# Kernel optimization log

Measured on AMD Instinct MI355X. Metric: run time of the kernel, lower is better.

Reference implementation:

```python
import jax, jax.numpy as jnp
import numpy as np

NUM_HEADS = 16
NEG = -1e9

def setup_inputs() -> dict:
    key = jax.random.key(0)
    ks = jax.random.split(key, 5)
    B, S, D = 4, 2048, 1024
    scale = 1.0 / np.sqrt(D)
    return {
        "x": jax.random.normal(ks[0], (B, S, D), dtype=jnp.float32),
        "WQ": jax.random.normal(ks[1], (D, D), dtype=jnp.float32) * scale,
        "WK": jax.random.normal(ks[2], (D, D), dtype=jnp.float32) * scale,
        "WV": jax.random.normal(ks[3], (D, D), dtype=jnp.float32) * scale,
        "WO": jax.random.normal(ks[4], (D, D), dtype=jnp.float32) * scale,
    }

def _split_heads(t, h):
    # [..., s, h*d] -> [..., h, s, d]
    *lead, s, hd = t.shape
    return jnp.swapaxes(t.reshape(*lead, s, h, hd // h), -3, -2)

def reference(x, WQ, WK, WV, WO):
    h = NUM_HEADS
    S = x.shape[-2]
    # Linear stores weight [out, in]; y = x @ W^T
    Q = _split_heads(x @ WQ.T, h)  # [b,h,s,dk]
    K = _split_heads(x @ WK.T, h)
    V = _split_heads(x @ WV.T, h)
    dk = Q.shape[-1]
    scores = jnp.einsum('bhqd,bhkd->bhqk', Q, K) / jnp.sqrt(jnp.float32(dk))
    causal = jnp.tril(jnp.ones((S, S), dtype=bool))  # allowed positions
    scores = jnp.where(causal, scores, NEG)
    # explicit stable softmax (matches source)
    m = jnp.max(scores, axis=-1, keepdims=True)
    e = jnp.exp(scores - m)
    attn = e / jnp.sum(e, axis=-1, keepdims=True)
    out = jnp.einsum('bhqk,bhkd->bhqd', attn, V)  # [b,h,s,dv]
    out = jnp.swapaxes(out, -3, -2).reshape(*x.shape[:-1], -1)  # [b,s,h*dv]
    return out @ WO.T
```

## Files before the change

kernel.cpp:

```cpp
#include <hip/hip_runtime.h>
#include <stdint.h>
#include <math.h>

typedef __attribute__((ext_vector_type(8))) short bf16x8;
typedef __attribute__((ext_vector_type(4))) short v4s;
typedef __attribute__((ext_vector_type(4))) float f32x4;
typedef __attribute__((ext_vector_type(4))) unsigned short u16x4;
typedef __attribute__((ext_vector_type(2))) unsigned int u32x2;

#define MFMA16(a,b,c)   __builtin_amdgcn_mfma_f32_16x16x32_bf16((a),(b),(c),0,0,0)
#define MFMA16K(a,b,c)  __builtin_amdgcn_mfma_f32_16x16x16bf16_1k((a),(b),(c),0,0,0)

static __device__ __forceinline__ void gld_lds16(const void* g, void* l) {
  __builtin_amdgcn_global_load_lds(
      (const __attribute__((address_space(1))) unsigned int*)g,
      (__attribute__((address_space(3))) unsigned int*)l,
      16, 0, 0);
}

static __device__ __forceinline__ unsigned short f2bf(float f) {
  unsigned int u = __builtin_bit_cast(unsigned int, f);
  return (unsigned short)((u + 0x8000u) >> 16);
}

__global__ __launch_bounds__(256) void cvt_kernel(const float* __restrict__ in,
                                                  unsigned short* __restrict__ out,
                                                  int n4) {
  int i = blockIdx.x * blockDim.x + threadIdx.x;
  int stride = gridDim.x * blockDim.x;
  for (; i < n4; i += stride) {
    float4 v = ((const float4*)in)[i];
    u16x4 o;
    o.x = f2bf(v.x); o.y = f2bf(v.y); o.z = f2bf(v.z); o.w = f2bf(v.w);
    ((u16x4*)out)[i] = o;
  }
}

__global__ __launch_bounds__(256) void cvt4_kernel(const float* __restrict__ w0,
                                                   const float* __restrict__ w1,
                                                   const float* __restrict__ w2,
                                                   const float* __restrict__ w3,
                                                   unsigned short* __restrict__ out) {
  const float* in = (blockIdx.y == 0) ? w0 : (blockIdx.y == 1) ? w1
                  : (blockIdx.y == 2) ? w2 : w3;
  unsigned short* o = out + (size_t)blockIdx.y * 1048576;
  int i = blockIdx.x * blockDim.x + threadIdx.x;
  int stride = gridDim.x * blockDim.x;
  for (; i < 1048576/4; i += stride) {
    float4 v = ((const float4*)in)[i];
    u16x4 t;
    t.x = f2bf(v.x); t.y = f2bf(v.y); t.z = f2bf(v.z); t.w = f2bf(v.w);
    ((u16x4*)o)[i] = t;
  }
}

template<int MODE, typename CT>
__device__ __forceinline__ void gemm_bt_tile(const unsigned short* __restrict__ A,
                                             const unsigned short* __restrict__ Bt,
                                             CT* __restrict__ C,
                                             int m0, int n0)
{
  __shared__ __align__(16) unsigned short As[128*32];
  __shared__ __align__(16) unsigned short Bs[128*32];
  const int tid  = threadIdx.x;
  const int w    = tid >> 6, lane = tid & 63;
  const int quad = lane >> 4, c0 = lane & 15;
  const int wm   = w >> 1, wn = w & 1;

  const unsigned short* ga[2];
  const unsigned short* gb[2];
  int ldsoff[2];
  #pragma unroll
  for (int i = 0; i < 2; ++i) {
    int f = i*4096 + w*1024 + lane*16;
    int r = f >> 6;
    int q = (f >> 4) & 3;
    ga[i] = A  + (m0 + r)*1024 + q*8;
    gb[i] = Bt + (n0 + r)*1024 + q*8;
    ldsoff[i] = i*4096 + w*1024;
  }

  int aAddr[4], bAddr[4];
  #pragma unroll
  for (int t = 0; t < 4; ++t) {
    aAddr[t] = (wm*64 + t*16 + c0)*64 + quad*16;
    bAddr[t] = (wn*64 + t*16 + c0)*64 + quad*16;
  }

  f32x4 acc[4][4];
  #pragma unroll
  for (int i = 0; i < 4; ++i)
    #pragma unroll
    for (int j = 0; j < 4; ++j)
      acc[i][j] = (f32x4){0.f, 0.f, 0.f, 0.f};

  for (int kt = 0; kt < 32; ++kt) {
    __syncthreads();
    #pragma unroll
    for (int i = 0; i < 2; ++i) {
      gld_lds16(ga[i] + kt*32, (char*)As + ldsoff[i]);
      gld_lds16(gb[i] + kt*32, (char*)Bs + ldsoff[i]);
    }
    __syncthreads();

    bf16x8 af[4], bfr[4];
    #pragma unroll
    for (int t = 0; t < 4; ++t) af[t]  = *(const bf16x8*)((const char*)As + aAddr[t]);
    #pragma unroll
    for (int t = 0; t < 4; ++t) bfr[t] = *(const bf16x8*)((const char*)Bs + bAddr[t]);

    #pragma unroll
    for (int mt = 0; mt < 4; ++mt)
      #pragma unroll
      for (int nt = 0; nt < 4; ++nt)
        acc[mt][nt] = MFMA16(af[mt], bfr[nt], acc[mt][nt]);
  }

  const float scl = (MODE == 3) ? 0.1803368801f : 1.0f;
  #pragma unroll
  for (int mt = 0; mt < 4; ++mt) {
    #pragma unroll
    for (int nt = 0; nt < 4; ++nt) {
      if (MODE == 2) {
        u16x4 pk;
        #pragma unroll
        for (int r = 0; r < 4; ++r) pk[r] = f2bf(acc[mt][nt][r]);
        int s0 = m0 + wm*64 + mt*16 + quad*4;
        int gc = n0 + wn*64 + nt*16 + c0;
        int b = s0 >> 11, ss = s0 & 2047;
        int h = gc >> 6, d = gc & 63;
        *(u16x4*)((unsigned short*)C + (size_t)(((b << 4) + h)*64 + d)*2048 + ss) = pk;
      } else {
        #pragma unroll
        for (int r = 0; r < 4; ++r) {
          int gr = m0 + wm*64 + mt*16 + quad*4 + r;
          int gc = n0 + wn*64 + nt*16 + c0;
          if (MODE == 0 || MODE == 3) {
            int b = gr >> 11, s = gr & 2047;
            int h = gc >> 6, d = gc & 63;
            ((unsigned short*)C)[(((b << 4) + h)*2048 + s)*64 + d] = f2bf(acc[mt][nt][r] * scl);
          } else {
            ((float*)C)[gr*1024 + gc] = acc[mt][nt][r];
          }
        }
      }
    }
  }
}

__global__ __launch_bounds__(256) void qkv_kernel(
    const unsigned short* __restrict__ X,
    const unsigned short* __restrict__ WQ, const unsigned short* __restrict__ WK,
    const unsigned short* __restrict__ WV,
    unsigned short* __restrict__ Q, unsigned short* __restrict__ K,
    unsigned short* __restrict__ V)
{
  if (blockIdx.z == 2) {
    gemm_bt_tile<2>(X, WV, V, blockIdx.x*128, blockIdx.y*128);
  } else if (blockIdx.z == 0) {
    gemm_bt_tile<3>(X, WQ, Q, blockIdx.x*128, blockIdx.y*128);
  } else {
    gemm_bt_tile<0>(X, WK, K, blockIdx.x*128, blockIdx.y*128);
  }
}

__global__ __launch_bounds__(256) void proj_kernel(
    const unsigned short* __restrict__ A,
    const unsigned short* __restrict__ WO,
    float* __restrict__ C)
{
  gemm_bt_tile<1>(A, WO, C, blockIdx.x*128, blockIdx.y*128);
}

__global__ __launch_bounds__(256) void attn_kernel(
    const unsigned short* __restrict__ Q,
    const unsigned short* __restrict__ K,
    const unsigned short* __restrict__ Vt,
    unsigned short* __restrict__ O)
{
  __shared__ __align__(16) unsigned short VtL[2][64*128];

  const int tid  = threadIdx.x;
  const int w    = tid >> 6, lane = tid & 63;
  const int quad = lane >> 4, c0 = lane & 15;
  const int bx = blockIdx.x, bh = blockIdx.y;

  const unsigned short* Qh = Q  + (size_t)bh*2048*64;
  const unsigned short* Kh = K  + (size_t)bh*2048*64;
  const unsigned short* Vh = Vt + (size_t)bh*64*2048;

  const unsigned short* vga[4];
  int vldsoff[4];
  #pragma unroll
  for (int i = 0; i < 4; ++i) {
    int cid = i*256 + tid;
    int r = cid >> 4, q = cid & 15;
    int gq = q ^ (r & 15);
    vga[i] = Vh + (size_t)r*2048 + gq*8;
    vldsoff[i] = i*4096 + w*1024;
  }

  const int b = bh >> 4, h = bh & 15;
  bf16x8 kreg[8][2];

  #define ATTN_MK_BODY(mk, Vb, DIAG)                                              \
  {                                                                               \
    f32x4 s0 = (f32x4){0.f,0.f,0.f,0.f}, s1 = (f32x4){0.f,0.f,0.f,0.f};           \
    _Pragma("unroll")                                                             \
    for (int ks = 0; ks < 2; ++ks) {                                              \
      s0 = MFMA16(kreg[mk][ks], qf[0][ks], s0);                                   \
      s1 = MFMA16(kreg[mk][ks], qf[1][ks], s1);                                   \
    }                                                                             \
    if (DIAG) {                                                                   \
      _Pragma("unroll")                                                           \
      for (int r = 0; r < 4; ++r) {                                               \
        int kk = (mk)*16 + quad*4 + r;                                            \
        if (kk > w*32 + c0)      s0[r] = -1e30f;                                  \
        if (kk > w*32 + 16 + c0) s1[r] = -1e30f;                                  \
      }                                                                           \
    }                                                                             \
    float p00 = __builtin_amdgcn_exp2f(s0[0]), p01 = __builtin_amdgcn_exp2f(s0[1]); \
    float p02 = __builtin_amdgcn_exp2f(s0[2]), p03 = __builtin_amdgcn_exp2f(s0[3]); \
    float p10 = __builtin_amdgcn_exp2f(s1[0]), p11 = __builtin_amdgcn_exp2f(s1[1]); \
    float p12 = __builtin_amdgcn_exp2f(s1[2]), p13 = __builtin_amdgcn_exp2f(s1[3]); \
    l_r[0] += (p00 + p01) + (p02 + p03);                                          \
    l_r[1] += (p10 + p11) + (p12 + p13);                                          \
    u32x2 a0, a1;                                                                 \
    a0.x = __builtin_amdgcn_perm(__builtin_bit_cast(unsigned int, p01),           \
                                 __builtin_bit_cast(unsigned int, p00), 0x07060302u); \
    a0.y = __builtin_amdgcn_perm(__builtin_bit_cast(unsigned int, p03),           \
                                 __builtin_bit_cast(unsigned int, p02), 0x07060302u); \
    a1.x = __builtin_amdgcn_perm(__builtin_bit_cast(unsigned int, p11),           \
                                 __builtin_bit_cast(unsigned int, p10), 0x07060302u); \
    a1.y = __builtin_amdgcn_perm(__builtin_bit_cast(unsigned int, p13),           \
                                 __builtin_bit_cast(unsigned int, p12), 0x07060302u); \
    v4s pa0 = __builtin_bit_cast(v4s, a0);                                        \
    v4s pa1 = __builtin_bit_cast(v4s, a1);                                        \
    _Pragma("unroll")                                                             \
    for (int dt = 0; dt < 4; ++dt) {                                              \
      int vr = dt*16 + c0;                                                        \
      int p  = 2*(mk) + (quad >> 1);                                              \
      v4s vb = *(const v4s*)((const char*)(Vb) + vr*256 + ((p ^ c0) * 16) + (quad & 1)*8); \
      o_[0][dt] = MFMA16K(pa0, vb, o_[0][dt]);                                    \
      o_[1][dt] = MFMA16K(pa1, vb, o_[1][dt]);                                    \
    }                                                                             \
  }

  for (int pi = 0; pi < 2; ++pi) {
    const int qt = pi ? bx : 15 - bx;

    bf16x8 qf[2][2];
    #pragma unroll
    for (int mq = 0; mq < 2; ++mq)
      #pragma unroll
      for (int ks = 0; ks < 2; ++ks)
        qf[mq][ks] = *(const bf16x8*)(Qh + (qt*128 + w*32 + mq*16 + c0)*64 + ks*32 + quad*8);

    f32x4 o_[2][4];
    float l_r[2] = {0.f, 0.f};
    #pragma unroll
    for (int mq = 0; mq < 2; ++mq)
      #pragma unroll
      for (int dt = 0; dt < 4; ++dt) o_[mq][dt] = (f32x4){0.f, 0.f, 0.f, 0.f};

    __syncthreads();
    #pragma unroll
    for (int i = 0; i < 4; ++i)
      gld_lds16(vga[i], (char*)VtL[0] + vldsoff[i]);
    #pragma unroll
    for (int mk = 0; mk < 8; ++mk)
      #pragma unroll
      for (int ks = 0; ks < 2; ++ks)
        kreg[mk][ks] = *(const bf16x8*)(Kh + (mk*16 + c0)*64 + ks*32 + quad*8);

    for (int kt = 0; kt < qt; ++kt) {
      __syncthreads();
      #pragma unroll
      for (int i = 0; i < 4; ++i)
        gld_lds16(vga[i] + (kt+1)*128, (char*)VtL[(kt+1)&1] + vldsoff[i]);
      const unsigned short* Vb = VtL[kt & 1];
      #pragma unroll
      for (int mk = 0; mk < 8; ++mk)
        ATTN_MK_BODY(mk, Vb, false)
      #pragma unroll
      for (int mk = 0; mk < 8; ++mk)
        #pragma unroll
        for (int ks = 0; ks < 2; ++ks)
          kreg[mk][ks] = *(const bf16x8*)(Kh + ((kt+1)*128 + mk*16 + c0)*64 + ks*32 + quad*8);
    }

    {
      __syncthreads();
      const unsigned short* Vb = VtL[qt & 1];
      #pragma unroll
      for (int mk = 0; mk < 8; ++mk)
        if (mk < 2*w + 2)
          ATTN_MK_BODY(mk, Vb, true)
    }

    #pragma unroll
    for (int mq = 0; mq < 2; ++mq) {
      l_r[mq] += __shfl_xor(l_r[mq], 16);
      l_r[mq] += __shfl_xor(l_r[mq], 32);
    }
    #pragma unroll
    for (int mt = 0; mt < 2; ++mt) {
      #pragma unroll
      for (int r = 0; r < 4; ++r) {
        float l = __shfl(l_r[mt], quad*4 + r);
        float inv = 1.0f / l;
        int srow = qt*128 + w*32 + mt*16 + quad*4 + r;
        #pragma unroll
        for (int dt = 0; dt < 4; ++dt) {
          int col = h*64 + dt*16 + c0;
          O[((size_t)b*2048 + srow)*1024 + col] = f2bf(o_[mt][dt][r] * inv);
        }
      }
    }
  }
  #undef ATTN_MK_BODY
}

extern "C" void kernel_launch(void* const* d_in, const int* in_sizes, int n_in,
                              void* d_out, int out_size, void* d_ws, size_t ws_size,
                              hipStream_t stream) {
  const float* xf  = (const float*)d_in[0];
  const float* wqf = (const float*)d_in[1];
  const float* wkf = (const float*)d_in[2];
  const float* wvf = (const float*)d_in[3];
  const float* wof = (const float*)d_in[4];
  float* out = (float*)d_out;
  unsigned short* ws = (unsigned short*)d_ws;

  const bool fused = ws_size >= (size_t)58720256;

  if (fused) {
    unsigned short* xb  = ws;
    unsigned short* wb  = ws + 8388608;
    unsigned short* Kw  = ws + 12582912;
    unsigned short* Vw  = ws + 20971520;
    unsigned short* Ow  = xb;
    unsigned short* Qd  = (unsigned short*)out;

    cvt_kernel <<<2048, 256, 0, stream>>>(xf, xb, 8388608/4);
    cvt4_kernel<<<dim3(256, 4), 256, 0, stream>>>(wqf, wkf, wvf, wof, wb);

    qkv_kernel <<<dim3(64, 8, 3), 256, 0, stream>>>(xb, wb, wb + 1048576, wb + 2097152,
                                                    Qd, Kw, Vw);
    attn_kernel<<<dim3(8, 64),    256, 0, stream>>>(Qd, Kw, Vw, Ow);
    proj_kernel<<<dim3(64, 8),    256, 0, stream>>>(Ow, wb + 3145728, out);
  } else {
    unsigned short* xb  = ws;
    unsigned short* wb  = ws + 8388608;
    unsigned short* Kw  = ws + 12582912;
    unsigned short* Vw  = ws + 14680064;
    unsigned short* Ow  = ws + 16777216;

    cvt_kernel <<<2048, 256, 0, stream>>>(xf, xb, 8388608/4);
    cvt4_kernel<<<dim3(256, 4), 256, 0, stream>>>(wqf, wkf, wvf, wof, wb);

    for (int b = 0; b < 4; ++b) {
      const unsigned short* xbb = xb  + (size_t)b * 2048 * 1024;
      float*               outb = out + (size_t)b * 2048 * 1024;
      unsigned short*        Qd = (unsigned short*)outb;
      qkv_kernel <<<dim3(16, 8, 3), 256, 0, stream>>>(xbb, wb, wb + 1048576, wb + 2097152,
                                                      Qd, Kw, Vw);
      attn_kernel<<<dim3(8, 16),    256, 0, stream>>>(Qd, Kw, Vw, Ow);
      proj_kernel<<<dim3(16, 8),    256, 0, stream>>>(Ow, wb + 3145728, outb);
    }
  }
}
```

Measured before the change: 265.6 us.

## Split attention query tile across 8 waves and interleave K prefetch

```diff
diff --git a/kernel.cpp b/kernel.cpp
--- a/kernel.cpp
+++ b/kernel.cpp
@@ -172,7 +172,7 @@
   gemm_bt_tile<1>(A, WO, C, blockIdx.x*128, blockIdx.y*128);
 }
 
-__global__ __launch_bounds__(256) void attn_kernel(
+__global__ __launch_bounds__(512, 4) void attn_kernel(
     const unsigned short* __restrict__ Q,
     const unsigned short* __restrict__ K,
     const unsigned short* __restrict__ Vt,
@@ -189,83 +189,72 @@
   const unsigned short* Kh = K  + (size_t)bh*2048*64;
   const unsigned short* Vh = Vt + (size_t)bh*64*2048;
 
-  const unsigned short* vga[4];
-  int vldsoff[4];
-  #pragma unroll
-  for (int i = 0; i < 4; ++i) {
-    int cid = i*256 + tid;
+  const unsigned short* vga[2];
+  int vldsoff[2];
+  #pragma unroll
+  for (int i = 0; i < 2; ++i) {
+    int cid = i*512 + tid;
     int r = cid >> 4, q = cid & 15;
     int gq = q ^ (r & 15);
     vga[i] = Vh + (size_t)r*2048 + gq*8;
-    vldsoff[i] = i*4096 + w*1024;
+    vldsoff[i] = i*8192 + w*1024;
   }
 
   const int b = bh >> 4, h = bh & 15;
   bf16x8 kreg[8][2];
 
-  #define ATTN_MK_BODY(mk, Vb, DIAG)                                              \
+  #define ATTN_MK_BODY(mk, Vb, DIAG, PF, kbase)                                   \
   {                                                                               \
-    f32x4 s0 = (f32x4){0.f,0.f,0.f,0.f}, s1 = (f32x4){0.f,0.f,0.f,0.f};           \
+    f32x4 s0 = (f32x4){0.f,0.f,0.f,0.f};                                          \
     _Pragma("unroll")                                                             \
-    for (int ks = 0; ks < 2; ++ks) {                                              \
-      s0 = MFMA16(kreg[mk][ks], qf[0][ks], s0);                                   \
-      s1 = MFMA16(kreg[mk][ks], qf[1][ks], s1);                                   \
+    for (int ks = 0; ks < 2; ++ks)                                                \
+      s0 = MFMA16(kreg[mk][ks], qf[ks], s0);                                      \
+    if (PF) {                                                                     \
+      _Pragma("unroll")                                                           \
+      for (int ks = 0; ks < 2; ++ks)                                              \
+        kreg[mk][ks] = *(const bf16x8*)((kbase) + ((mk)*16 + c0)*64 + ks*32 + quad*8); \
     }                                                                             \
     if (DIAG) {                                                                   \
       _Pragma("unroll")                                                           \
       for (int r = 0; r < 4; ++r) {                                               \
         int kk = (mk)*16 + quad*4 + r;                                            \
-        if (kk > w*32 + c0)      s0[r] = -1e30f;                                  \
-        if (kk > w*32 + 16 + c0) s1[r] = -1e30f;                                  \
+        if (kk > w*16 + c0) s0[r] = -1e30f;                                       \
       }                                                                           \
     }                                                                             \
     float p00 = __builtin_amdgcn_exp2f(s0[0]), p01 = __builtin_amdgcn_exp2f(s0[1]); \
     float p02 = __builtin_amdgcn_exp2f(s0[2]), p03 = __builtin_amdgcn_exp2f(s0[3]); \
-    float p10 = __builtin_amdgcn_exp2f(s1[0]), p11 = __builtin_amdgcn_exp2f(s1[1]); \
-    float p12 = __builtin_amdgcn_exp2f(s1[2]), p13 = __builtin_amdgcn_exp2f(s1[3]); \
-    l_r[0] += (p00 + p01) + (p02 + p03);                                          \
-    l_r[1] += (p10 + p11) + (p12 + p13);                                          \
-    u32x2 a0, a1;                                                                 \
+    l_r += (p00 + p01) + (p02 + p03);                                             \
+    u32x2 a0;                                                                     \
     a0.x = __builtin_amdgcn_perm(__builtin_bit_cast(unsigned int, p01),           \
                                  __builtin_bit_cast(unsigned int, p00), 0x07060302u); \
     a0.y = __builtin_amdgcn_perm(__builtin_bit_cast(unsigned int, p03),           \
                                  __builtin_bit_cast(unsigned int, p02), 0x07060302u); \
-    a1.x = __builtin_amdgcn_perm(__builtin_bit_cast(unsigned int, p11),           \
-                                 __builtin_bit_cast(unsigned int, p10), 0x07060302u); \
-    a1.y = __builtin_amdgcn_perm(__builtin_bit_cast(unsigned int, p13),           \
-                                 __builtin_bit_cast(unsigned int, p12), 0x07060302u); \
     v4s pa0 = __builtin_bit_cast(v4s, a0);                                        \
-    v4s pa1 = __builtin_bit_cast(v4s, a1);                                        \
     _Pragma("unroll")                                                             \
     for (int dt = 0; dt < 4; ++dt) {                                              \
       int vr = dt*16 + c0;                                                        \
       int p  = 2*(mk) + (quad >> 1);                                              \
       v4s vb = *(const v4s*)((const char*)(Vb) + vr*256 + ((p ^ c0) * 16) + (quad & 1)*8); \
-      o_[0][dt] = MFMA16K(pa0, vb, o_[0][dt]);                                    \
-      o_[1][dt] = MFMA16K(pa1, vb, o_[1][dt]);                                    \
+      o_[dt] = MFMA16K(pa0, vb, o_[dt]);                                          \
     }                                                                             \
   }
 
   for (int pi = 0; pi < 2; ++pi) {
     const int qt = pi ? bx : 15 - bx;
 
-    bf16x8 qf[2][2];
-    #pragma unroll
-    for (int mq = 0; mq < 2; ++mq)
-      #pragma unroll
-      for (int ks = 0; ks < 2; ++ks)
-        qf[mq][ks] = *(const bf16x8*)(Qh + (qt*128 + w*32 + mq*16 + c0)*64 + ks*32 + quad*8);
-
-    f32x4 o_[2][4];
-    float l_r[2] = {0.f, 0.f};
-    #pragma unroll
-    for (int mq = 0; mq < 2; ++mq)
-      #pragma unroll
-      for (int dt = 0; dt < 4; ++dt) o_[mq][dt] = (f32x4){0.f, 0.f, 0.f, 0.f};
+    bf16x8 qf[2];
+    #pragma unroll
+    for (int ks = 0; ks < 2; ++ks)
+      qf[ks] = *(const bf16x8*)(Qh + (qt*128 + w*16 + c0)*64 + ks*32 + quad*8);
+
+    f32x4 o_[4];
+    float l_r = 0.f;
+    #pragma unroll
+    for (int dt = 0; dt < 4; ++dt) o_[dt] = (f32x4){0.f, 0.f, 0.f, 0.f};
 
     __syncthreads();
     #pragma unroll
-    for (int i = 0; i < 4; ++i)
+    for (int i = 0; i < 2; ++i)
       gld_lds16(vga[i], (char*)VtL[0] + vldsoff[i]);
     #pragma unroll
     for (int mk = 0; mk < 8; ++mk)
@@ -276,17 +265,13 @@
     for (int kt = 0; kt < qt; ++kt) {
       __syncthreads();
       #pragma unroll
-      for (int i = 0; i < 4; ++i)
+      for (int i = 0; i < 2; ++i)
         gld_lds16(vga[i] + (kt+1)*128, (char*)VtL[(kt+1)&1] + vldsoff[i]);
       const unsigned short* Vb = VtL[kt & 1];
+      const unsigned short* Kn = Kh + (kt+1)*128*64;
       #pragma unroll
       for (int mk = 0; mk < 8; ++mk)
-        ATTN_MK_BODY(mk, Vb, false)
-      #pragma unroll
-      for (int mk = 0; mk < 8; ++mk)
-        #pragma unroll
-        for (int ks = 0; ks < 2; ++ks)
-          kreg[mk][ks] = *(const bf16x8*)(Kh + ((kt+1)*128 + mk*16 + c0)*64 + ks*32 + quad*8);
+        ATTN_MK_BODY(mk, Vb, false, true, Kn)
     }
 
     {
@@ -294,27 +279,21 @@
       const unsigned short* Vb = VtL[qt & 1];
       #pragma unroll
       for (int mk = 0; mk < 8; ++mk)
-        if (mk < 2*w + 2)
-          ATTN_MK_BODY(mk, Vb, true)
-    }
-
-    #pragma unroll
-    for (int mq = 0; mq < 2; ++mq) {
-      l_r[mq] += __shfl_xor(l_r[mq], 16);
-      l_r[mq] += __shfl_xor(l_r[mq], 32);
-    }
-    #pragma unroll
-    for (int mt = 0; mt < 2; ++mt) {
-      #pragma unroll
-      for (int r = 0; r < 4; ++r) {
-        float l = __shfl(l_r[mt], quad*4 + r);
-        float inv = 1.0f / l;
-        int srow = qt*128 + w*32 + mt*16 + quad*4 + r;
-        #pragma unroll
-        for (int dt = 0; dt < 4; ++dt) {
-          int col = h*64 + dt*16 + c0;
-          O[((size_t)b*2048 + srow)*1024 + col] = f2bf(o_[mt][dt][r] * inv);
-        }
+        if (mk <= w)
+          ATTN_MK_BODY(mk, Vb, true, false, Kh)
+    }
+
+    l_r += __shfl_xor(l_r, 16);
+    l_r += __shfl_xor(l_r, 32);
+    #pragma unroll
+    for (int r = 0; r < 4; ++r) {
+      float l = __shfl(l_r, quad*4 + r);
+      float inv = 1.0f / l;
+      int srow = qt*128 + w*16 + quad*4 + r;
+      #pragma unroll
+      for (int dt = 0; dt < 4; ++dt) {
+        int col = h*64 + dt*16 + c0;
+        O[((size_t)b*2048 + srow)*1024 + col] = f2bf(o_[dt][r] * inv);
       }
     }
   }
@@ -347,7 +326,7 @@
 
     qkv_kernel <<<dim3(64, 8, 3), 256, 0, stream>>>(xb, wb, wb + 1048576, wb + 2097152,
                                                     Qd, Kw, Vw);
-    attn_kernel<<<dim3(8, 64),    256, 0, stream>>>(Qd, Kw, Vw, Ow);
+    attn_kernel<<<dim3(8, 64),    512, 0, stream>>>(Qd, Kw, Vw, Ow);
     proj_kernel<<<dim3(64, 8),    256, 0, stream>>>(Ow, wb + 3145728, out);
   } else {
     unsigned short* xb  = ws;
@@ -365,7 +344,7 @@
       unsigned short*        Qd = (unsigned short*)outb;
       qkv_kernel <<<dim3(16, 8, 3), 256, 0, stream>>>(xbb, wb, wb + 1048576, wb + 2097152,
                                                       Qd, Kw, Vw);
-      attn_kernel<<<dim3(8, 16),    256, 0, stream>>>(Qd, Kw, Vw, Ow);
+      attn_kernel<<<dim3(8, 16),    512, 0, stream>>>(Qd, Kw, Vw, Ow);
       proj_kernel<<<dim3(16, 8),    256, 0, stream>>>(Ow, wb + 3145728, outb);
     }
   }
```

After: 350.9 us. 32.1% more time.
